# Kernel tuning notes

Hardware: AMD Instinct MI355X
Metric: run time of the kernel (lower is better)

Reference implementation:

```python
import jax, jax.numpy as jnp
import numpy as np

N_NODES = 50000
N_EDGES = 800000
IN_FEATS = 96
HIDDEN = 96
OUT_FEATS = 8


def setup_inputs() -> dict:
    key = jax.random.key(0)
    k = jax.random.split(key, 10)
    features = jax.random.normal(k[0], (N_NODES, IN_FEATS), dtype=jnp.float32)
    src = jax.random.randint(k[1], (N_EDGES,), 0, N_NODES, dtype=jnp.int32)
    dst = jax.random.randint(k[2], (N_EDGES,), 0, N_NODES, dtype=jnp.int32)
    # DGL GraphConv weights: shape (in, out), xavier-uniform; bias zeros (we use small randn for nontrivial grads)
    def glorot(kk, fan_in, fan_out):
        lim = np.sqrt(6.0 / (fan_in + fan_out))
        return jax.random.uniform(kk, (fan_in, fan_out), jnp.float32, -lim, lim)
    W1 = glorot(k[3], IN_FEATS, HIDDEN)
    b1 = jnp.zeros((HIDDEN,), jnp.float32)
    W2 = glorot(k[4], HIDDEN, HIDDEN)
    b2 = jnp.zeros((HIDDEN,), jnp.float32)
    # torch Linear readout: weight [out, in], bias [out]
    Wr = glorot(k[5], OUT_FEATS, HIDDEN)
    br = jnp.zeros((OUT_FEATS,), jnp.float32)
    return {"features": features, "src": src, "dst": dst,
            "W1": W1, "b1": b1, "W2": W2, "b2": b2, "Wr": Wr, "br": br}


def _degree_norms(src, dst, n_nodes):
    ones = jnp.ones(src.shape[0], jnp.float32)
    deg_out = jax.ops.segment_sum(ones, src, num_segments=n_nodes)
    deg_in = jax.ops.segment_sum(ones, dst, num_segments=n_nodes)
    norm_out = jnp.clip(deg_out, 1.0, None) ** -0.5  # D_out^{-1/2}
    norm_in = jnp.clip(deg_in, 1.0, None) ** -0.5    # D_in^{-1/2}
    return norm_out, norm_in


def _graph_conv(x, src, dst, norm_out, norm_in, W, b):
    # DGL GraphConv, norm='both': scale src feats, sum-aggregate over edges,
    # scale by in-degree norm, dense transform + bias.
    x = x * norm_out[:, None]
    msgs = x[src]                                           # [E, d] gather
    agg = jax.ops.segment_sum(msgs, dst, num_segments=x.shape[0])  # [N, d] scatter-add
    agg = agg * norm_in[:, None]
    return agg @ W + b


def reference(features, src, dst, W1, b1, W2, b2, Wr, br):
    n = features.shape[0]
    norm_out, norm_in = _degree_norms(src, dst, n)
    x = jax.nn.relu(_graph_conv(features, src, dst, norm_out, norm_in, W1, b1))
    x = _graph_conv(x, src, dst, norm_out, norm_in, W2, b2)
    hg = jnp.mean(x, axis=0, keepdims=True)  # [1, hidden]
    return hg @ Wr.T + br                    # [1, out_feats]
```

## Files before the change

### kernel.cpp

```cpp
#include <hip/hip_runtime.h>


constexpr int NN = 50000;
constexpr int NE = 800000;
constexpr int NB = 196;
constexpr int CAP = 6144;

constexpr int OFF_SVEC     = 0;
constexpr int OFF_BCURD    = 256;
constexpr int OFF_BCURS    = 3392;
constexpr int OFF_NORM_OUT = 6528;
constexpr int OFF_NORM_IN  = 56528;
constexpr int OFF_CW       = 106528;
constexpr int OFF_ROW_PTR  = 156528;
constexpr int OFF_EDGE_SRC = 206532;
constexpr int OFF_PD       = 606532;
constexpr int OFF_PS       = 1810756;
constexpr int OFF_YP       = 606532;
constexpr size_t ZERO_BYTES = (size_t)(OFF_NORM_OUT) * 4;

__global__ __launch_bounds__(256)
void k_part(const int* __restrict__ src, const int* __restrict__ dst,
            int* __restrict__ bcur_d, int* __restrict__ bcur_s,
            int* __restrict__ pd, int* __restrict__ ps) {
  __shared__ int hd[256], hs[256], gd[256], gs[256];
  __shared__ int ldx[256], cur[256], scn[256];
  __shared__ int stage[2048];
  __shared__ unsigned char stageB[2048];
  const int t = threadIdx.x;
  hd[t] = 0; hs[t] = 0;
  __syncthreads();
  const int e0 = blockIdx.x * 2048;
  int s_[8], d_[8];
#pragma unroll
  for (int i = 0; i < 8; ++i) {
    int e = e0 + i * 256 + t;
    bool v = e < NE;
    s_[i] = v ? src[e] : -1;
    d_[i] = v ? dst[e] : -1;
    if (v) { atomicAdd(&hd[d_[i] >> 8], 1); atomicAdd(&hs[s_[i] >> 8], 1); }
  }
  __syncthreads();
  if (t < NB) {
    int c = hd[t];
    gd[t] = c ? (t * CAP + atomicAdd(&bcur_d[t * 16], c)) : 0;
    c = hs[t];
    gs[t] = c ? (t * CAP + atomicAdd(&bcur_s[t * 16], c)) : 0;
  }

  scn[t] = hd[t];
  __syncthreads();
  for (int off = 1; off < 256; off <<= 1) {
    int u = (t >= off) ? scn[t - off] : 0;
    __syncthreads();
    scn[t] += u;
    __syncthreads();
  }
  ldx[t] = scn[t] - hd[t];
  cur[t] = scn[t] - hd[t];
  const int totd = scn[255];
  __syncthreads();
#pragma unroll
  for (int i = 0; i < 8; ++i) {
    if (d_[i] >= 0) {
      int B = d_[i] >> 8;
      int p = atomicAdd(&cur[B], 1);
      stage[p] = (s_[i] << 8) | (d_[i] & 255);
      stageB[p] = (unsigned char)B;
    }
  }
  __syncthreads();
  for (int j = t; j < totd; j += 256) {
    int B = stageB[j];
    pd[gd[B] + (j - ldx[B])] = stage[j];
  }
  __syncthreads();

  scn[t] = hs[t];
  __syncthreads();
  for (int off = 1; off < 256; off <<= 1) {
    int u = (t >= off) ? scn[t - off] : 0;
    __syncthreads();
    scn[t] += u;
    __syncthreads();
  }
  ldx[t] = scn[t] - hs[t];
  cur[t] = scn[t] - hs[t];
  const int tots = scn[255];
  __syncthreads();
#pragma unroll
  for (int i = 0; i < 8; ++i) {
    if (s_[i] >= 0) {
      int B = s_[i] >> 8;
      int p = atomicAdd(&cur[B], 1);
      stage[p] = (d_[i] << 8) | (s_[i] & 255);
      stageB[p] = (unsigned char)B;
    }
  }
  __syncthreads();
  for (int j = t; j < tots; j += 256) {
    int B = stageB[j];
    ps[gs[B] + (j - ldx[B])] = stage[j];
  }
}

__global__ __launch_bounds__(256)
void k_csr(const int* __restrict__ pd, const int* __restrict__ bcur_d,
           int* __restrict__ row_ptr, float* __restrict__ norm_in,
           unsigned short* __restrict__ edge_src) {
  __shared__ int pe_s[CAP];
  __shared__ int hist[256], cur[256], sc[256];
  const int t = threadIdx.x, b = blockIdx.x;
  hist[t] = 0;
  __syncthreads();
  const int cnt = bcur_d[b * 16];
  const int* pe = pd + b * CAP;
  for (int i = t; i < cnt; i += 256) {
    int p = pe[i];
    pe_s[i] = p;
    atomicAdd(&hist[p & 255], 1);
  }

  sc[t] = (t < b) ? bcur_d[t * 16] : 0;
  __syncthreads();
  for (int s = 128; s > 0; s >>= 1) {
    if (t < s) sc[t] += sc[t + s];
    __syncthreads();
  }
  const int base0 = sc[0];
  __syncthreads();

  int h = hist[t];
  sc[t] = h;
  __syncthreads();
  for (int off = 1; off < 256; off <<= 1) {
    int u = (t >= off) ? sc[t - off] : 0;
    __syncthreads();
    sc[t] += u;
    __syncthreads();
  }
  int excl = base0 + sc[t] - h;
  int n = b * 256 + t;
  if (n < NN) {
    row_ptr[n] = excl;
    norm_in[n] = 1.0f / sqrtf((float)max(h, 1));
  }
  cur[t] = excl;
  __syncthreads();
  if (b == NB - 1 && t == 0) row_ptr[NN] = base0 + cnt;

  for (int i = t; i < cnt; i += 256) {
    int p = pe_s[i];
    int pos = atomicAdd(&cur[p & 255], 1);
    edge_src[pos] = (unsigned short)(p >> 8);
  }
}

__global__ __launch_bounds__(256)
void k_bin_src(const int* __restrict__ ps, const int* __restrict__ bcur_s,
               const float* __restrict__ norm_in,
               float* __restrict__ norm_out, float* __restrict__ cw) {
  __shared__ int dout[256];
  __shared__ float craw[256];
  const int t = threadIdx.x, b = blockIdx.x;
  dout[t] = 0; craw[t] = 0.f;
  __syncthreads();
  const int cnt = bcur_s[b * 16];
  const int* pe = ps + b * CAP;
  for (int i = t; i < cnt; i += 256) {
    int p = pe[i];
    atomicAdd(&dout[p & 255], 1);
    atomicAdd(&craw[p & 255], norm_in[p >> 8]);
  }
  __syncthreads();
  int n = b * 256 + t;
  if (n < NN) {
    float no = 1.0f / sqrtf((float)max(dout[t], 1));
    norm_out[n] = no;
    cw[n] = no * craw[t];
  }
}

__global__ __launch_bounds__(256, 6)
void k_xform(const float* __restrict__ feats, const float* __restrict__ norm_out,
             const float* __restrict__ W1, float* __restrict__ YP) {
  __shared__ float XT[96][68];
  const int t = threadIdx.x;
  const int nb = blockIdx.x * 64;

  const float4* f4 = (const float4*)feats;
#pragma unroll
  for (int i = 0; i < 6; ++i) {
    int idx4 = i * 256 + t;
    int n = idx4 / 24;
    int kq = idx4 % 24;
    int ng = nb + n;
    float4 v = make_float4(0.f, 0.f, 0.f, 0.f);
    float no = 0.f;
    if (ng < NN) { v = f4[(size_t)ng * 24 + kq]; no = norm_out[ng]; }
    XT[kq * 4 + 0][n] = v.x * no;
    XT[kq * 4 + 1][n] = v.y * no;
    XT[kq * 4 + 2][n] = v.z * no;
    XT[kq * 4 + 3][n] = v.w * no;
  }
  __syncthreads();

  const int tn = t & 7;
  const int tm = t >> 3;
  float acc0[12], acc1[12];
#pragma unroll
  for (int c = 0; c < 12; ++c) { acc0[c] = 0.f; acc1[c] = 0.f; }

  const float4* W4 = (const float4*)(W1 + 12 * tn);
#pragma unroll 4
  for (int k = 0; k < 96; ++k) {
    float2 x = *(const float2*)&XT[k][2 * tm];
    float4 w0 = W4[k * 24 + 0];
    float4 w1 = W4[k * 24 + 1];
    float4 w2 = W4[k * 24 + 2];
    const float w[12] = {w0.x, w0.y, w0.z, w0.w, w1.x, w1.y, w1.z, w1.w,
                         w2.x, w2.y, w2.z, w2.w};
#pragma unroll
    for (int c = 0; c < 12; ++c) {
      acc0[c] = fmaf(x.x, w[c], acc0[c]);
      acc1[c] = fmaf(x.y, w[c], acc1[c]);
    }
  }

  int n0 = nb + 2 * tm;
  if (n0 < NN) {
    float4* yp = (float4*)(YP + ((size_t)tn * NN + n0) * 12);
    yp[0] = make_float4(acc0[0], acc0[1], acc0[2], acc0[3]);
    yp[1] = make_float4(acc0[4], acc0[5], acc0[6], acc0[7]);
    yp[2] = make_float4(acc0[8], acc0[9], acc0[10], acc0[11]);
  }
  if (n0 + 1 < NN) {
    float4* yp = (float4*)(YP + ((size_t)tn * NN + n0 + 1) * 12);
    yp[0] = make_float4(acc1[0], acc1[1], acc1[2], acc1[3]);
    yp[1] = make_float4(acc1[4], acc1[5], acc1[6], acc1[7]);
    yp[2] = make_float4(acc1[8], acc1[9], acc1[10], acc1[11]);
  }
}

__global__ __launch_bounds__(256, 6)
void k_agg(const float* __restrict__ YP,
           const float* __restrict__ norm_in, const float* __restrict__ cw,
           const int* __restrict__ row_ptr, const unsigned short* __restrict__ edge_src,
           const float* __restrict__ b1, float* __restrict__ svec) {
  __shared__ float red[12];
  const int tid = threadIdx.x;
  if (tid < 12) red[tid] = 0.f;
  __syncthreads();

  const int panel = blockIdx.x & 7;
  const int bp    = blockIdx.x >> 3;
  const int g = tid >> 5, l = tid & 31;
  const int ei = l / 3;
  const int q4 = (l - 3 * ei) * 4;
  const bool act = (l < 24);

  const float* Yp = YP + (size_t)panel * NN * 12;
  float4 b4 = make_float4(0.f, 0.f, 0.f, 0.f);
  if (l < 3) b4 = ((const float4*)b1)[3 * panel + l];

  float a0 = 0.f, a1 = 0.f, a2 = 0.f, a3 = 0.f;

  const int gid = bp * 8 + g;
  for (int n = gid; n < NN; n += 4096) {
    const int m = n + 2048;
    const bool hb = (m < NN);
    int e1a = row_ptr[n + 1], basea = row_ptr[n];
    int e1b = 0, baseb = 0;
    if (hb) { e1b = row_ptr[m + 1]; baseb = row_ptr[m]; }
    float va0 = 0.f, va1 = 0.f, va2 = 0.f, va3 = 0.f;
    float vb0 = 0.f, vb1 = 0.f, vb2 = 0.f, vb3 = 0.f;

    while (basea < e1a || baseb < e1b) {
      int cnta = min(32, e1a - basea);
      int cntb = min(32, e1b - baseb);
      int esa = 0, esb = 0;
      if (basea + l < e1a) esa = edge_src[basea + l] * 12;
      if (baseb + l < e1b) esb = edge_src[baseb + l] * 12;

      if (cnta > 0) {
        int s0 = __shfl(esa, ei, 32);
        float4 f0 = make_float4(0.f, 0.f, 0.f, 0.f);
        if (act && ei < cnta) f0 = *(const float4*)(Yp + s0 + q4);
        if (cnta > 8) {
          int s1 = __shfl(esa, 8 + ei, 32);
          float4 f1 = make_float4(0.f, 0.f, 0.f, 0.f);
          if (act && 8 + ei < cnta) f1 = *(const float4*)(Yp + s1 + q4);
          f0.x += f1.x; f0.y += f1.y; f0.z += f1.z; f0.w += f1.w;
        }
        if (cnta > 16) {
          int s2 = __shfl(esa, 16 + ei, 32);
          int s3 = __shfl(esa, 24 + ei, 32);
          float4 f2 = make_float4(0.f, 0.f, 0.f, 0.f), f3 = f2;
          if (act && 16 + ei < cnta) f2 = *(const float4*)(Yp + s2 + q4);
          if (act && 24 + ei < cnta) f3 = *(const float4*)(Yp + s3 + q4);
          f0.x += f2.x + f3.x; f0.y += f2.y + f3.y;
          f0.z += f2.z + f3.z; f0.w += f2.w + f3.w;
        }
        va0 += f0.x; va1 += f0.y; va2 += f0.z; va3 += f0.w;
      }
      if (cntb > 0) {
        int s0 = __shfl(esb, ei, 32);
        float4 f0 = make_float4(0.f, 0.f, 0.f, 0.f);
        if (act && ei < cntb) f0 = *(const float4*)(Yp + s0 + q4);
        if (cntb > 8) {
          int s1 = __shfl(esb, 8 + ei, 32);
          float4 f1 = make_float4(0.f, 0.f, 0.f, 0.f);
          if (act && 8 + ei < cntb) f1 = *(const float4*)(Yp + s1 + q4);
          f0.x += f1.x; f0.y += f1.y; f0.z += f1.z; f0.w += f1.w;
        }
        if (cntb > 16) {
          int s2 = __shfl(esb, 16 + ei, 32);
          int s3 = __shfl(esb, 24 + ei, 32);
          float4 f2 = make_float4(0.f, 0.f, 0.f, 0.f), f3 = f2;
          if (act && 16 + ei < cntb) f2 = *(const float4*)(Yp + s2 + q4);
          if (act && 24 + ei < cntb) f3 = *(const float4*)(Yp + s3 + q4);
          f0.x += f2.x + f3.x; f0.y += f2.y + f3.y;
          f0.z += f2.z + f3.z; f0.w += f2.w + f3.w;
        }
        vb0 += f0.x; vb1 += f0.y; vb2 += f0.z; vb3 += f0.w;
      }
      basea += 32; baseb += 32;
    }

    va0 += __shfl(va0, l + 12, 32); va1 += __shfl(va1, l + 12, 32);
    va2 += __shfl(va2, l + 12, 32); va3 += __shfl(va3, l + 12, 32);
    va0 += __shfl(va0, l + 6, 32);  va1 += __shfl(va1, l + 6, 32);
    va2 += __shfl(va2, l + 6, 32);  va3 += __shfl(va3, l + 6, 32);
    va0 += __shfl(va0, l + 3, 32);  va1 += __shfl(va1, l + 3, 32);
    va2 += __shfl(va2, l + 3, 32);  va3 += __shfl(va3, l + 3, 32);

    vb0 += __shfl(vb0, l + 12, 32); vb1 += __shfl(vb1, l + 12, 32);
    vb2 += __shfl(vb2, l + 12, 32); vb3 += __shfl(vb3, l + 12, 32);
    vb0 += __shfl(vb0, l + 6, 32);  vb1 += __shfl(vb1, l + 6, 32);
    vb2 += __shfl(vb2, l + 6, 32);  vb3 += __shfl(vb3, l + 6, 32);
    vb0 += __shfl(vb0, l + 3, 32);  vb1 += __shfl(vb1, l + 3, 32);
    vb2 += __shfl(vb2, l + 3, 32);  vb3 += __shfl(vb3, l + 3, 32);

    if (l < 3) {
      float ni = norm_in[n], c = cw[n];
      a0 += c * fmaxf(fmaf(ni, va0, b4.x), 0.f);
      a1 += c * fmaxf(fmaf(ni, va1, b4.y), 0.f);
      a2 += c * fmaxf(fmaf(ni, va2, b4.z), 0.f);
      a3 += c * fmaxf(fmaf(ni, va3, b4.w), 0.f);
      if (hb) {
        float nib = norm_in[m], cb = cw[m];
        a0 += cb * fmaxf(fmaf(nib, vb0, b4.x), 0.f);
        a1 += cb * fmaxf(fmaf(nib, vb1, b4.y), 0.f);
        a2 += cb * fmaxf(fmaf(nib, vb2, b4.z), 0.f);
        a3 += cb * fmaxf(fmaf(nib, vb3, b4.w), 0.f);
      }
    }
  }

  if (l < 3) {
    atomicAdd(&red[4 * l + 0], a0);
    atomicAdd(&red[4 * l + 1], a1);
    atomicAdd(&red[4 * l + 2], a2);
    atomicAdd(&red[4 * l + 3], a3);
  }
  __syncthreads();
  if (tid < 12) atomicAdd(&svec[12 * panel + tid], red[tid]);
}

__global__ void k_final(const float* __restrict__ svec,
                        const float* __restrict__ W2, const float* __restrict__ b2,
                        const float* __restrict__ Wr, const float* __restrict__ br,
                        float* __restrict__ out) {
  __shared__ float hg[96];
  int j = threadIdx.x;
  if (j < 96) {
    float acc = b2[j];
    const float invN = 1.0f / (float)NN;
    for (int k = 0; k < 96; ++k)
      acc = fmaf(svec[k] * invN, W2[k * 96 + j], acc);
    hg[j] = acc;
  }
  __syncthreads();
  if (j < 8) {
    float acc = br[j];
    for (int k = 0; k < 96; ++k)
      acc = fmaf(hg[k], Wr[j * 96 + k], acc);
    out[j] = acc;
  }
}

extern "C" void kernel_launch(void* const* d_in, const int* in_sizes, int n_in,
                              void* d_out, int out_size, void* d_ws, size_t ws_size,
                              hipStream_t stream) {
  const float* feats = (const float*)d_in[0];
  const int*   src   = (const int*)d_in[1];
  const int*   dst   = (const int*)d_in[2];
  const float* W1    = (const float*)d_in[3];
  const float* b1    = (const float*)d_in[4];
  const float* W2    = (const float*)d_in[5];
  const float* b2    = (const float*)d_in[6];
  const float* Wr    = (const float*)d_in[7];
  const float* br    = (const float*)d_in[8];
  float* out = (float*)d_out;

  int*   wsi      = (int*)d_ws;
  float* wsf      = (float*)d_ws;
  float* svec     = wsf + OFF_SVEC;
  int*   bcur_d   = wsi + OFF_BCURD;
  int*   bcur_s   = wsi + OFF_BCURS;
  float* norm_out = wsf + OFF_NORM_OUT;
  float* norm_in  = wsf + OFF_NORM_IN;
  float* cw       = wsf + OFF_CW;
  int*   row_ptr  = wsi + OFF_ROW_PTR;
  unsigned short* edge_src = (unsigned short*)(wsi + OFF_EDGE_SRC);
  int*   pd       = wsi + OFF_PD;
  int*   ps       = wsi + OFF_PS;
  float* YP       = wsf + OFF_YP;

  hipMemsetAsync(d_ws, 0, ZERO_BYTES, stream);

  k_part<<<(NE + 2047) / 2048, 256, 0, stream>>>(src, dst, bcur_d, bcur_s, pd, ps);
  k_csr<<<NB, 256, 0, stream>>>(pd, bcur_d, row_ptr, norm_in, edge_src);
  k_bin_src<<<NB, 256, 0, stream>>>(ps, bcur_s, norm_in, norm_out, cw);
  k_xform<<<(NN + 63) / 64, 256, 0, stream>>>(feats, norm_out, W1, YP);
  k_agg<<<2048, 256, 0, stream>>>(YP, norm_in, cw, row_ptr, edge_src, b1, svec);
  k_final<<<1, 128, 0, stream>>>(svec, W2, b2, Wr, br, out);
}
```

Measured before the change: 219.5 us.

## Repack projected features into six 16-column panels with uneven XCD assignment

Changes the intermediate YP layout from eight 12-float panels to six 16-float (64-byte) panels, so each gathered row uses all 32 lanes as 8 edges × 4 float4 with no idle lanes. The aggregation kernel maps the 8 XCD-interleaved block groups onto 6 panels, giving panels 0 and 1 two XCDs each with a split node range, so per-XCD working sets stay in L2. This aims to raise gather efficiency and cut the number of panel passes over the edge list, at the cost of an uneven work split and a larger working set per panel.

New measurement: 219.7 us. No clear change (+0.1%).

```diff
diff --git a/kernel.cpp b/kernel.cpp
--- a/kernel.cpp
+++ b/kernel.cpp
@@ -228,17 +228,17 @@
   }
 
   int n0 = nb + 2 * tm;
-  if (n0 < NN) {
-    float4* yp = (float4*)(YP + ((size_t)tn * NN + n0) * 12);
-    yp[0] = make_float4(acc0[0], acc0[1], acc0[2], acc0[3]);
-    yp[1] = make_float4(acc0[4], acc0[5], acc0[6], acc0[7]);
-    yp[2] = make_float4(acc0[8], acc0[9], acc0[10], acc0[11]);
-  }
-  if (n0 + 1 < NN) {
-    float4* yp = (float4*)(YP + ((size_t)tn * NN + n0 + 1) * 12);
-    yp[0] = make_float4(acc1[0], acc1[1], acc1[2], acc1[3]);
-    yp[1] = make_float4(acc1[4], acc1[5], acc1[6], acc1[7]);
-    yp[2] = make_float4(acc1[8], acc1[9], acc1[10], acc1[11]);
+#pragma unroll
+  for (int c4 = 0; c4 < 3; ++c4) {
+    int col = 12 * tn + 4 * c4;
+    int p = col >> 4, off = col & 15;
+    float* base = YP + ((size_t)p * NN) * 16 + off;
+    if (n0 < NN)
+      *(float4*)(base + (size_t)n0 * 16) =
+          make_float4(acc0[4 * c4], acc0[4 * c4 + 1], acc0[4 * c4 + 2], acc0[4 * c4 + 3]);
+    if (n0 + 1 < NN)
+      *(float4*)(base + (size_t)(n0 + 1) * 16) =
+          make_float4(acc1[4 * c4], acc1[4 * c4 + 1], acc1[4 * c4 + 2], acc1[4 * c4 + 3]);
   }
 }
 
@@ -247,27 +247,31 @@
            const float* __restrict__ norm_in, const float* __restrict__ cw,
            const int* __restrict__ row_ptr, const unsigned short* __restrict__ edge_src,
            const float* __restrict__ b1, float* __restrict__ svec) {
-  __shared__ float red[12];
+  __shared__ float red[16];
   const int tid = threadIdx.x;
-  if (tid < 12) red[tid] = 0.f;
-  __syncthreads();
-
-  const int panel = blockIdx.x & 7;
+  if (tid < 16) red[tid] = 0.f;
+  __syncthreads();
+
+  const int xcd   = blockIdx.x & 7;
   const int bp    = blockIdx.x >> 3;
+  const int panel = (xcd < 6) ? xcd : (xcd - 6);
+  const int slotb = (xcd >= 6) ? 256 : 0;
+  const int nslot = (panel < 2) ? 512 : 256;
+  const int stride = nslot * 8;
+
   const int g = tid >> 5, l = tid & 31;
-  const int ei = l / 3;
-  const int q4 = (l - 3 * ei) * 4;
-  const bool act = (l < 24);
-
-  const float* Yp = YP + (size_t)panel * NN * 12;
+  const int ei = l >> 2;
+  const int q4 = (l & 3) * 4;
+
+  const float* Yp = YP + (size_t)panel * NN * 16;
   float4 b4 = make_float4(0.f, 0.f, 0.f, 0.f);
-  if (l < 3) b4 = ((const float4*)b1)[3 * panel + l];
+  if (l < 4) b4 = ((const float4*)b1)[4 * panel + l];
 
   float a0 = 0.f, a1 = 0.f, a2 = 0.f, a3 = 0.f;
 
-  const int gid = bp * 8 + g;
-  for (int n = gid; n < NN; n += 4096) {
-    const int m = n + 2048;
+  const int gid = (slotb + bp) * 8 + g;
+  for (int n = gid; n < NN; n += 2 * stride) {
+    const int m = n + stride;
     const bool hb = (m < NN);
     int e1a = row_ptr[n + 1], basea = row_ptr[n];
     int e1b = 0, baseb = 0;
@@ -279,25 +283,25 @@
       int cnta = min(32, e1a - basea);
       int cntb = min(32, e1b - baseb);
       int esa = 0, esb = 0;
-      if (basea + l < e1a) esa = edge_src[basea + l] * 12;
-      if (baseb + l < e1b) esb = edge_src[baseb + l] * 12;
+      if (basea + l < e1a) esa = edge_src[basea + l] * 16;
+      if (baseb + l < e1b) esb = edge_src[baseb + l] * 16;
 
       if (cnta > 0) {
         int s0 = __shfl(esa, ei, 32);
         float4 f0 = make_float4(0.f, 0.f, 0.f, 0.f);
-        if (act && ei < cnta) f0 = *(const float4*)(Yp + s0 + q4);
+        if (ei < cnta) f0 = *(const float4*)(Yp + s0 + q4);
         if (cnta > 8) {
           int s1 = __shfl(esa, 8 + ei, 32);
           float4 f1 = make_float4(0.f, 0.f, 0.f, 0.f);
-          if (act && 8 + ei < cnta) f1 = *(const float4*)(Yp + s1 + q4);
+          if (8 + ei < cnta) f1 = *(const float4*)(Yp + s1 + q4);
           f0.x += f1.x; f0.y += f1.y; f0.z += f1.z; f0.w += f1.w;
         }
         if (cnta > 16) {
           int s2 = __shfl(esa, 16 + ei, 32);
           int s3 = __shfl(esa, 24 + ei, 32);
           float4 f2 = make_float4(0.f, 0.f, 0.f, 0.f), f3 = f2;
-          if (act && 16 + ei < cnta) f2 = *(const float4*)(Yp + s2 + q4);
-          if (act && 24 + ei < cnta) f3 = *(const float4*)(Yp + s3 + q4);
+          if (16 + ei < cnta) f2 = *(const float4*)(Yp + s2 + q4);
+          if (24 + ei < cnta) f3 = *(const float4*)(Yp + s3 + q4);
           f0.x += f2.x + f3.x; f0.y += f2.y + f3.y;
           f0.z += f2.z + f3.z; f0.w += f2.w + f3.w;
         }
@@ -306,19 +310,19 @@
       if (cntb > 0) {
         int s0 = __shfl(esb, ei, 32);
         float4 f0 = make_float4(0.f, 0.f, 0.f, 0.f);
-        if (act && ei < cntb) f0 = *(const float4*)(Yp + s0 + q4);
+        if (ei < cntb) f0 = *(const float4*)(Yp + s0 + q4);
         if (cntb > 8) {
           int s1 = __shfl(esb, 8 + ei, 32);
           float4 f1 = make_float4(0.f, 0.f, 0.f, 0.f);
-          if (act && 8 + ei < cntb) f1 = *(const float4*)(Yp + s1 + q4);
+          if (8 + ei < cntb) f1 = *(const float4*)(Yp + s1 + q4);
           f0.x += f1.x; f0.y += f1.y; f0.z += f1.z; f0.w += f1.w;
         }
         if (cntb > 16) {
           int s2 = __shfl(esb, 16 + ei, 32);
           int s3 = __shfl(esb, 24 + ei, 32);
           float4 f2 = make_float4(0.f, 0.f, 0.f, 0.f), f3 = f2;
-          if (act && 16 + ei < cntb) f2 = *(const float4*)(Yp + s2 + q4);
-          if (act && 24 + ei < cntb) f3 = *(const float4*)(Yp + s3 + q4);
+          if (16 + ei < cntb) f2 = *(const float4*)(Yp + s2 + q4);
+          if (24 + ei < cntb) f3 = *(const float4*)(Yp + s3 + q4);
           f0.x += f2.x + f3.x; f0.y += f2.y + f3.y;
           f0.z += f2.z + f3.z; f0.w += f2.w + f3.w;
         }
@@ -327,21 +331,21 @@
       basea += 32; baseb += 32;
     }
 
-    va0 += __shfl(va0, l + 12, 32); va1 += __shfl(va1, l + 12, 32);
-    va2 += __shfl(va2, l + 12, 32); va3 += __shfl(va3, l + 12, 32);
-    va0 += __shfl(va0, l + 6, 32);  va1 += __shfl(va1, l + 6, 32);
-    va2 += __shfl(va2, l + 6, 32);  va3 += __shfl(va3, l + 6, 32);
-    va0 += __shfl(va0, l + 3, 32);  va1 += __shfl(va1, l + 3, 32);
-    va2 += __shfl(va2, l + 3, 32);  va3 += __shfl(va3, l + 3, 32);
-
-    vb0 += __shfl(vb0, l + 12, 32); vb1 += __shfl(vb1, l + 12, 32);
-    vb2 += __shfl(vb2, l + 12, 32); vb3 += __shfl(vb3, l + 12, 32);
-    vb0 += __shfl(vb0, l + 6, 32);  vb1 += __shfl(vb1, l + 6, 32);
-    vb2 += __shfl(vb2, l + 6, 32);  vb3 += __shfl(vb3, l + 6, 32);
-    vb0 += __shfl(vb0, l + 3, 32);  vb1 += __shfl(vb1, l + 3, 32);
-    vb2 += __shfl(vb2, l + 3, 32);  vb3 += __shfl(vb3, l + 3, 32);
-
-    if (l < 3) {
+    va0 += __shfl(va0, l + 16, 32); va1 += __shfl(va1, l + 16, 32);
+    va2 += __shfl(va2, l + 16, 32); va3 += __shfl(va3, l + 16, 32);
+    va0 += __shfl(va0, l + 8, 32);  va1 += __shfl(va1, l + 8, 32);
+    va2 += __shfl(va2, l + 8, 32);  va3 += __shfl(va3, l + 8, 32);
+    va0 += __shfl(va0, l + 4, 32);  va1 += __shfl(va1, l + 4, 32);
+    va2 += __shfl(va2, l + 4, 32);  va3 += __shfl(va3, l + 4, 32);
+
+    vb0 += __shfl(vb0, l + 16, 32); vb1 += __shfl(vb1, l + 16, 32);
+    vb2 += __shfl(vb2, l + 16, 32); vb3 += __shfl(vb3, l + 16, 32);
+    vb0 += __shfl(vb0, l + 8, 32);  vb1 += __shfl(vb1, l + 8, 32);
+    vb2 += __shfl(vb2, l + 8, 32);  vb3 += __shfl(vb3, l + 8, 32);
+    vb0 += __shfl(vb0, l + 4, 32);  vb1 += __shfl(vb1, l + 4, 32);
+    vb2 += __shfl(vb2, l + 4, 32);  vb3 += __shfl(vb3, l + 4, 32);
+
+    if (l < 4) {
       float ni = norm_in[n], c = cw[n];
       a0 += c * fmaxf(fmaf(ni, va0, b4.x), 0.f);
       a1 += c * fmaxf(fmaf(ni, va1, b4.y), 0.f);
@@ -357,14 +361,14 @@
     }
   }
 
-  if (l < 3) {
+  if (l < 4) {
     atomicAdd(&red[4 * l + 0], a0);
     atomicAdd(&red[4 * l + 1], a1);
     atomicAdd(&red[4 * l + 2], a2);
     atomicAdd(&red[4 * l + 3], a3);
   }
   __syncthreads();
-  if (tid < 12) atomicAdd(&svec[12 * panel + tid], red[tid]);
+  if (tid < 16) atomicAdd(&svec[16 * panel + tid], red[tid]);
 }
 
 __global__ void k_final(const float* __restrict__ svec,
```
